# Kernel optimization log

Measured on AMD Instinct MI355X. Metric: run time of the kernel, lower is better.

The kernel has to match this reference:

```python
import math
import jax, jax.numpy as jnp
import numpy as np
from jax import lax

B, T, C, H = 8, 2048, 1024, 16
E = C // H
FACTOR = 5
TOP_K = int(FACTOR * math.log(T))  # 38


def setup_inputs() -> dict:
    key = jax.random.key(0)
    ks = jax.random.split(key, 9)
    s = 1.0 / math.sqrt(C)
    return {
        "x": jax.random.normal(ks[0], (B, T, C), dtype=jnp.float32),
        "Wq": jax.random.normal(ks[1], (C, C), dtype=jnp.float32) * s,
        "bq": jnp.zeros((C,), dtype=jnp.float32),
        "Wk": jax.random.normal(ks[2], (C, C), dtype=jnp.float32) * s,
        "bk": jnp.zeros((C,), dtype=jnp.float32),
        "Wv": jax.random.normal(ks[3], (C, C), dtype=jnp.float32) * s,
        "bv": jnp.zeros((C,), dtype=jnp.float32),
        "Wp": jax.random.normal(ks[4], (C, C), dtype=jnp.float32) * s,
        "bp": jnp.zeros((C,), dtype=jnp.float32),
    }


def _autocorrelation(x, Wq, bq, Wk, bk, Wv, bv, Wp, bp):
    # Q, K, V projections -> [B, T, H, E]
    q = (x @ Wq + bq).reshape(B, T, H, E)
    k = (x @ Wk + bk).reshape(B, T, H, E)
    v = (x @ Wv + bv).reshape(B, T, H, E)

    # [B, H, E, L] layout for FFT along time axis
    qh = q.transpose(0, 2, 3, 1)
    kh = k.transpose(0, 2, 3, 1)
    values = v.transpose(0, 2, 3, 1)

    # period-based dependency discovery via FFT cross-correlation
    qf = jnp.fft.rfft(qh, axis=-1)
    kf = jnp.fft.rfft(kh, axis=-1)
    corr = jnp.fft.irfft(qf * jnp.conj(kf), n=T, axis=-1)  # [B, H, E, L]

    # inference-mode time-delay aggregation (per-batch top-k delays)
    mean_value = jnp.mean(corr, axis=(1, 2))               # [B, L]
    weights, delay = lax.top_k(mean_value, TOP_K)          # [B, K] each
    tmp_corr = jax.nn.softmax(weights, axis=-1)            # [B, K]

    init_index = jnp.arange(T)

    def step(agg, wd):
        w, d = wd  # w: [B], d: [B]  (one delay per batch element)
        idx = (init_index[None, :] + d[:, None]) % T        # modular roll == gather on doubled values
        pattern = jnp.take_along_axis(values, idx[:, None, None, :], axis=-1)
        return agg + pattern * w[:, None, None, None], None

    agg, _ = lax.scan(step, jnp.zeros_like(values),
                      (tmp_corr.T, delay.T))               # [B, H, E, L]

    # Faithful to the original: permute(0,3,1,2) then transpose(1,2) then view(B,T,C)
    # net effect: [B,H,E,L] -> [B,H,L,E] -> reshape(B,T,C)
    V = agg.transpose(0, 1, 3, 2).reshape(B, T, C)
    return V @ Wp + bp  # dropouts are inactive (eval mode)


def reference(x, Wq, bq, Wk, bk, Wv, bv, Wp, bp):
    return _autocorrelation(x, Wq, bq, Wk, bk, Wv, bv, Wp, bp)
```

## Files before the change

### kernel.cpp

```cpp
#include <hip/hip_runtime.h>

#define T_LEN 2048
#define B_DIM 8
#define C_DIM 1024
#define TOPK  38
#define FFT_N 2048
#define SPEC_ST 2050

typedef _Float16 half8 __attribute__((ext_vector_type(8)));
typedef _Float16 half4 __attribute__((ext_vector_type(4)));
typedef float  floatx4 __attribute__((ext_vector_type(4)));
typedef unsigned int u32;

__device__ __forceinline__ void async16(const void* g, void* l) {
  __builtin_amdgcn_global_load_lds(
      (const __attribute__((address_space(1))) u32*)g,
      (__attribute__((address_space(3))) u32*)l, 16, 0, 0);
}

__device__ __forceinline__ int rev11(int x) { return (int)(__brev((u32)x) >> 21); }
__device__ __forceinline__ int SW(int a) { return a ^ ((a >> 5) & 31); }

struct cpx { float r, i; };
__device__ __forceinline__ cpx csqr(cpx a) { return {a.r*a.r - a.i*a.i, 2.0f*a.r*a.i}; }
__device__ __forceinline__ cpx c8m(cpx a, int m) {
  const float R2 = 0.70710678118654752f;
  switch (m & 3) {
    case 0:  return a;
    case 1:  return {R2*(a.r + a.i), R2*(a.i - a.r)};
    case 2:  return {a.i, -a.r};
    default: return {R2*(a.i - a.r), -R2*(a.r + a.i)};
  }
}

__device__ __forceinline__ void radix8(float zr[8], float zi[8], cpx tb) {
  cpx tb2 = csqr(tb), tb4 = csqr(tb2);
  #pragma unroll
  for (int m = 0; m < 4; ++m) {
    cpx tw = c8m(tb, m);
    float ur = zr[m], ui = zi[m], vr = zr[m+4], vi = zi[m+4];
    zr[m] = ur + vr; zi[m] = ui + vi;
    float sr = ur - vr, si = ui - vi;
    zr[m+4] = sr*tw.r - si*tw.i; zi[m+4] = sr*tw.i + si*tw.r;
  }
  cpx twb = c8m(tb2, 2);
  #pragma unroll
  for (int h = 0; h < 2; ++h) {
    int b0 = h * 4;
    { cpx tw = tb2;
      float ur = zr[b0], ui = zi[b0], vr = zr[b0+2], vi = zi[b0+2];
      zr[b0] = ur + vr; zi[b0] = ui + vi;
      float sr = ur - vr, si = ui - vi;
      zr[b0+2] = sr*tw.r - si*tw.i; zi[b0+2] = sr*tw.i + si*tw.r; }
    { cpx tw = twb;
      float ur = zr[b0+1], ui = zi[b0+1], vr = zr[b0+3], vi = zi[b0+3];
      zr[b0+1] = ur + vr; zi[b0+1] = ui + vi;
      float sr = ur - vr, si = ui - vi;
      zr[b0+3] = sr*tw.r - si*tw.i; zi[b0+3] = sr*tw.i + si*tw.r; }
  }
  #pragma unroll
  for (int p = 0; p < 8; p += 2) {
    float ur = zr[p], ui = zi[p], vr = zr[p+1], vi = zi[p+1];
    zr[p] = ur + vr; zi[p] = ui + vi;
    float sr = ur - vr, si = ui - vi;
    zr[p+1] = sr*tb4.r - si*tb4.i; zi[p+1] = sr*tb4.i + si*tb4.r;
  }
}

__global__ __launch_bounds__(256) void init_kernel(
    float* __restrict__ spec, int n, float* __restrict__ twg) {
  int i = blockIdx.x * 256 + threadIdx.x;
  if (i < n) spec[i] = 0.0f;
  if (i < FFT_N / 2) {
    float th = -3.14159265358979323846f * (float)i / 1024.0f;
    twg[2 * i]     = cosf(th);
    twg[2 * i + 1] = sinf(th);
  }
}

__global__ __launch_bounds__(256) void cvt_f16_kernel(
    const float* __restrict__ src, _Float16* __restrict__ dst, int n8) {
  int i = blockIdx.x * 256 + threadIdx.x;
  if (i >= n8) return;
  floatx4 a = ((const floatx4*)src)[i * 2];
  floatx4 b = ((const floatx4*)src)[i * 2 + 1];
  half8 o;
  #pragma unroll
  for (int j = 0; j < 4; ++j) { o[j] = (_Float16)a[j]; o[j + 4] = (_Float16)b[j]; }
  ((half8*)dst)[i] = o;
}

__global__ __launch_bounds__(256) void wt3_kernel(
    const float* __restrict__ w0, const float* __restrict__ w1,
    const float* __restrict__ w2, _Float16* __restrict__ d0,
    _Float16* __restrict__ d1, _Float16* __restrict__ d2) {
  const float* src = blockIdx.z == 0 ? w0 : (blockIdx.z == 1 ? w1 : w2);
  _Float16*    dst = blockIdx.z == 0 ? d0 : (blockIdx.z == 1 ? d1 : d2);
  __shared__ _Float16 tile[64][65];
  int k0 = blockIdx.y * 64, n0 = blockIdx.x * 64;
  int tx = threadIdx.x & 63, ty = threadIdx.x >> 6;
  #pragma unroll
  for (int j = 0; j < 16; ++j) {
    int r = j * 4 + ty;
    tile[r][tx] = (_Float16)src[(size_t)(k0 + r) * C_DIM + n0 + tx];
  }
  __syncthreads();
  #pragma unroll
  for (int j = 0; j < 16; ++j) {
    int r = j * 4 + ty;
    dst[(size_t)(n0 + r) * C_DIM + k0 + tx] = tile[tx][r];
  }
}

__global__ __launch_bounds__(256) void tr16_kernel(
    const _Float16* __restrict__ src, _Float16* __restrict__ dst) {
  __shared__ _Float16 tile[64][65];
  int b = blockIdx.z;
  int t0 = blockIdx.x * 64, c0 = blockIdx.y * 64;
  const _Float16* s = src + (size_t)b * T_LEN * C_DIM;
  _Float16* d = dst + (size_t)b * C_DIM * T_LEN;
  int tid = threadIdx.x;
  int c8 = (tid & 7) * 8, tr = tid >> 3;
  #pragma unroll
  for (int h = 0; h < 2; ++h) {
    int r = tr + h * 32;
    half8 v = *(const half8*)&s[(size_t)(t0 + r) * C_DIM + c0 + c8];
    #pragma unroll
    for (int j = 0; j < 8; ++j) tile[r][c8 + j] = v[j];
  }
  __syncthreads();
  int t8 = (tid & 7) * 8, cr = tid >> 3;
  #pragma unroll
  for (int h = 0; h < 2; ++h) {
    int c = cr + h * 32;
    half8 o;
    #pragma unroll
    for (int j = 0; j < 8; ++j) o[j] = tile[t8 + j][c];
    *(half8*)&d[(size_t)(c0 + c) * T_LEN + t0 + t8] = o;
  }
}

#define CG 4
__global__ __launch_bounds__(256) void fft_corr_kernel(
    const _Float16* __restrict__ XMt, const _Float16* __restrict__ Xt,
    const float* __restrict__ twg, float* __restrict__ spec) {
  __shared__ float2 zc[FFT_N];
  const int tid = threadIdx.x;
  const int b = blockIdx.x & 7;
  const int cg0 = (blockIdx.x >> 3) * CG;
  const int lo5 = tid & 31, blk = tid >> 5;
  const int lo2 = tid & 3,  g   = tid >> 2;
  const _Float16* xmB = XMt + (size_t)b * C_DIM * T_LEN;
  const _Float16* xB  = Xt  + (size_t)b * C_DIM * T_LEN;
  float sRa[4] = {0.f, 0.f, 0.f, 0.f};
  float sIa[4] = {0.f, 0.f, 0.f, 0.f};
  float s1024 = 0.f;
  float zr[8], zi[8], nr[8], ni[8];
  #pragma unroll
  for (int m = 0; m < 8; ++m) {
    nr[m] = (float)xmB[(size_t)cg0 * T_LEN + tid + 256 * m];
    ni[m] = (float)xB [(size_t)cg0 * T_LEN + tid + 256 * m];
  }
  cpx tA = {twg[2 * tid],            twg[2 * tid + 1]};
  cpx tB = {twg[2 * (8 * lo5)],      twg[2 * (8 * lo5) + 1]};
  cpx tC = {twg[2 * (64 * lo2)],     twg[2 * (64 * lo2) + 1]};
  for (int cc = 0; cc < CG; ++cc) {
    #pragma unroll
    for (int m = 0; m < 8; ++m) { zr[m] = nr[m]; zi[m] = ni[m]; }
    if (cc + 1 < CG) {
      const size_t off = (size_t)(cg0 + cc + 1) * T_LEN;
      #pragma unroll
      for (int m = 0; m < 8; ++m) {
        nr[m] = (float)xmB[off + tid + 256 * m];
        ni[m] = (float)xB [off + tid + 256 * m];
      }
    }
    radix8(zr, zi, tA);
    __syncthreads();
    #pragma unroll
    for (int m = 0; m < 8; ++m) { int a = SW(tid + 256 * m); zc[a] = make_float2(zr[m], zi[m]); }
    __syncthreads();
    #pragma unroll
    for (int m = 0; m < 8; ++m) { float2 v = zc[SW(256 * blk + 32 * m + lo5)]; zr[m] = v.x; zi[m] = v.y; }
    radix8(zr, zi, tB);
    __syncthreads();
    #pragma unroll
    for (int m = 0; m < 8; ++m) { int a = SW(256 * blk + 32 * m + lo5); zc[a] = make_float2(zr[m], zi[m]); }
    __syncthreads();
    #pragma unroll
    for (int m = 0; m < 8; ++m) { float2 v = zc[SW(32 * g + 4 * m + lo2)]; zr[m] = v.x; zi[m] = v.y; }
    radix8(zr, zi, tC);
    #pragma unroll
    for (int m = 0; m < 8; ++m) {
      float pr = __shfl_xor(zr[m], 2), pi = __shfl_xor(zi[m], 2);
      if ((tid & 2) == 0) { zr[m] += pr; zi[m] += pi; }
      else {
        float sr = pr - zr[m], si = pi - zi[m];
        if (tid & 1) { zr[m] = si; zi[m] = -sr; }
        else         { zr[m] = sr; zi[m] = si; }
      }
    }
    #pragma unroll
    for (int m = 0; m < 8; ++m) {
      float pr = __shfl_xor(zr[m], 1), pi = __shfl_xor(zi[m], 1);
      if ((tid & 1) == 0) { zr[m] += pr; zi[m] += pi; }
      else                { zr[m] = pr - zr[m]; zi[m] = pi - zi[m]; }
    }
    __syncthreads();
    #pragma unroll
    for (int m = 0; m < 8; ++m) { int a = SW(32 * g + 4 * m + lo2); zc[a] = make_float2(zr[m], zi[m]); }
    __syncthreads();
    #pragma unroll
    for (int r = 0; r < 4; ++r) {
      int k = tid + r * 256;
      if (k == 0) {
        float2 z0 = zc[SW(0)], z1 = zc[SW(1)];
        sRa[0] += z0.x * z0.y;
        s1024  += z1.x * z1.y;
      } else {
        float2 zk = zc[SW(rev11(k))], zn = zc[SW(rev11(FFT_N - k))];
        float ar = 0.5f * (zk.x + zn.x), ai = 0.5f * (zk.y - zn.y);
        float br = 0.5f * (zk.y + zn.y), bi = -0.5f * (zk.x - zn.x);
        sRa[r] += ar * br + ai * bi;
        sIa[r] += ai * br - ar * bi;
      }
    }
  }
  float* sb = spec + (size_t)b * SPEC_ST;
  #pragma unroll
  for (int r = 0; r < 4; ++r) {
    int k = tid + r * 256;
    atomicAdd(&sb[2 * k],     sRa[r]);
    atomicAdd(&sb[2 * k + 1], sIa[r]);
  }
  if (tid == 0) atomicAdd(&sb[2048], s1024);
}

__global__ __launch_bounds__(256) void ifft_topk_kernel(
    const float* __restrict__ spec, const float* __restrict__ twg,
    float* __restrict__ wgt, int* __restrict__ dly) {
  __shared__ float re[FFT_N], im[FFT_N];
  __shared__ float twr[FFT_N / 2], twi[FFT_N / 2];
  __shared__ float vals[FFT_N];
  __shared__ float swv[4];
  __shared__ int   swidx[4];
  __shared__ float selw[TOPK];
  __shared__ int   seli[TOPK];
  int b = blockIdx.x, tid = threadIdx.x;
  for (int i = tid; i < FFT_N / 2; i += 256) { twr[SW(i)] = twg[2 * i]; twi[SW(i)] = twg[2 * i + 1]; }
  const float* sb = spec + (size_t)b * SPEC_ST;
  for (int i = tid; i < FFT_N; i += 256) {
    int src = (i <= 1024) ? i : (FFT_N - i);
    float sgn = (i <= 1024) ? 1.0f : -1.0f;
    re[SW(i)] = sb[2 * src];
    im[SW(i)] = sgn * sb[2 * src + 1];
  }
  __syncthreads();
  #pragma unroll 1
  for (int s = 0; s < 11; ++s) {
    const int half = 1024 >> s, tstep = 1 << s;
    #pragma unroll
    for (int r = 0; r < 4; ++r) {
      int idx = tid + r * 256;
      int j = idx & (half - 1);
      int i0 = SW(2 * idx - j), i1 = SW(2 * idx - j + half);
      float ur = re[i0], ui = im[i0], vr = re[i1], vi = im[i1];
      float sr = ur - vr, si = ui - vi;
      int tix = SW(j * tstep);
      float wr = twr[tix], wi = twi[tix];
      re[i0] = ur + vr; im[i0] = ui + vi;
      re[i1] = sr * wr + si * wi;
      im[i1] = si * wr - sr * wi;
    }
    __syncthreads();
  }
  const float sc = 1.0f / 2097152.0f;
  for (int i = tid; i < FFT_N; i += 256) vals[SW(rev11(i))] = re[SW(i)] * sc;
  __syncthreads();
  for (int it = 0; it < TOPK; ++it) {
    float bv = -3.4e38f; int bi = T_LEN - 1;
    for (int i = tid; i < T_LEN; i += 256) {
      float v = vals[SW(i)];
      if (v > bv || (v == bv && i < bi)) { bv = v; bi = i; }
    }
    #pragma unroll
    for (int off = 32; off > 0; off >>= 1) {
      float ov = __shfl_down(bv, off);
      int   oi = __shfl_down(bi, off);
      if (ov > bv || (ov == bv && oi < bi)) { bv = ov; bi = oi; }
    }
    if ((tid & 63) == 0) { swv[tid >> 6] = bv; swidx[tid >> 6] = bi; }
    __syncthreads();
    if (tid == 0) {
      #pragma unroll
      for (int ww = 1; ww < 4; ++ww) {
        float ov = swv[ww]; int oi = swidx[ww];
        if (ov > bv || (ov == bv && oi < bi)) { bv = ov; bi = oi; }
      }
      if (bi < 0) bi = 0; if (bi > T_LEN - 1) bi = T_LEN - 1;
      selw[it] = bv; seli[it] = bi;
      vals[SW(bi)] = -3.4e38f;
    }
    __syncthreads();
  }
  if (tid == 0) {
    float m = selw[0], s = 0.0f, e[TOPK];
    for (int i = 0; i < TOPK; ++i) { e[i] = expf(selw[i] - m); s += e[i]; }
    float inv = 1.0f / s;
    for (int i = 0; i < TOPK; ++i) { wgt[b * TOPK + i] = e[i] * inv; dly[b * TOPK + i] = seli[i]; }
  }
}

template <int EPI>
__global__ __launch_bounds__(256, 3) void gemm_f16_kernel(
    const _Float16* __restrict__ A, const _Float16* __restrict__ B,
    const float* __restrict__ bias, void* __restrict__ outv, int N, int K,
    const _Float16* __restrict__ B2, const float* __restrict__ bias2,
    void* __restrict__ outv2) {
  __shared__ __align__(16) _Float16 lA[128 * 64];
  __shared__ __align__(16) _Float16 lB[128 * 64];

  if (blockIdx.z) { B = B2; bias = bias2; outv = outv2; }

  const int tid = threadIdx.x;
  const int bm = blockIdx.x, bn = blockIdx.y;
  const int lane = tid & 63, w = tid >> 6;
  const int wm = w >> 1, wn = w & 1;
  const int lr = lane & 15, lg = lane >> 4;

  const int lrow = lane >> 3;
  const int lcol = (((lane & 7) ^ lrow) * 8);

  const _Float16* pA[4];
  const _Float16* pB[4];
  _Float16* dA[4];
  _Float16* dB[4];
  #pragma unroll
  for (int j = 0; j < 4; ++j) {
    int r = w * 32 + j * 8;
    pA[j] = A + (long long)(bm * 128 + r + lrow) * K + lcol;
    pB[j] = B + (long long)(bn * 128 + r + lrow) * K + lcol;
    dA[j] = &lA[r * 64];
    dB[j] = &lB[r * 64];
  }

  const int coff = (((lr >> 2) & 1) * 32) | ((lg ^ (lr & 3)) * 8);

  floatx4 acc[4][4];
  #pragma unroll
  for (int i = 0; i < 4; ++i)
    #pragma unroll
    for (int j = 0; j < 4; ++j) { acc[i][j][0]=0.f; acc[i][j][1]=0.f; acc[i][j][2]=0.f; acc[i][j][3]=0.f; }

  const int nk = K >> 6;
  for (int kt = 0; kt < nk; ++kt) {
    __syncthreads();
    #pragma unroll
    for (int j = 0; j < 4; ++j) {
      async16(pA[j], dA[j]);
      async16(pB[j], dB[j]);
      pA[j] += 64; pB[j] += 64;
    }
    __syncthreads();
    #pragma unroll
    for (int s = 0; s < 2; ++s) {
      const int so = coff ^ (s * 32);
      half8 af[4], bf[4];
      #pragma unroll
      for (int mi = 0; mi < 4; ++mi)
        af[mi] = *(const half8*)&lA[(wm * 64 + mi * 16 + lr) * 64 + so];
      #pragma unroll
      for (int ni = 0; ni < 4; ++ni)
        bf[ni] = *(const half8*)&lB[(wn * 64 + ni * 16 + lr) * 64 + so];
      #pragma unroll
      for (int mi = 0; mi < 4; ++mi)
        #pragma unroll
        for (int ni = 0; ni < 4; ++ni)
          acc[mi][ni] = __builtin_amdgcn_mfma_f32_16x16x32_f16(
              af[mi], bf[ni], acc[mi][ni], 0, 0, 0);
    }
  }

  if (EPI == 2 && blockIdx.z == 0) {
    #pragma unroll
    for (int mi = 0; mi < 4; ++mi)
      #pragma unroll
      for (int ni = 0; ni < 4; ++ni) {
        int gc  = bn * 128 + wn * 64 + ni * 16 + lr;
        int gr0 = bm * 128 + wm * 64 + mi * 16 + lg * 4;
        int bb = gr0 >> 11, t0 = gr0 & (T_LEN - 1);
        half4 o;
        #pragma unroll
        for (int i = 0; i < 4; ++i) o[i] = (_Float16)acc[mi][ni][i];
        *(half4*)&(((_Float16*)outv)[((size_t)bb * C_DIM + gc) * T_LEN + t0]) = o;
      }
    return;
  }

  float bvs[4];
  #pragma unroll
  for (int ni = 0; ni < 4; ++ni) {
    int gc = bn * 128 + wn * 64 + ni * 16 + lr;
    bvs[ni] = bias ? bias[gc & (C_DIM - 1)] : 0.0f;
  }
  #pragma unroll
  for (int mi = 0; mi < 4; ++mi)
    #pragma unroll
    for (int ni = 0; ni < 4; ++ni) {
      int gc = bn * 128 + wn * 64 + ni * 16 + lr;
      #pragma unroll
      for (int i = 0; i < 4; ++i) {
        int gr = bm * 128 + wm * 64 + mi * 16 + lg * 4 + i;
        float v = acc[mi][ni][i] + bvs[ni];
        long long idx = (long long)gr * N + gc;
        if constexpr (EPI == 1) ((float*)outv)[idx] = v;
        else                    ((_Float16*)outv)[idx] = (_Float16)v;
      }
    }
}

__global__ __launch_bounds__(256) void aggregate_kernel(
    const _Float16* __restrict__ V, const float* __restrict__ wgt,
    const int* __restrict__ dly, _Float16* __restrict__ V2) {
  int b = blockIdx.x & 7;
  int g = (blockIdx.x >> 3) * 256 + threadIdx.x;
  int c8 = g & 127;
  int tp = g >> 7;
  int h = tp >> 7, lhi = tp & 127;
  int cp = c8 << 3;
  int e0 = cp & 63, lo = cp >> 6;
  int l = lhi * 16 + lo;
  int ch = h * 64 + e0;
  float acc[8];
  #pragma unroll
  for (int j = 0; j < 8; ++j) acc[j] = 0.0f;
  const long long vbase = (long long)b * T_LEN * C_DIM;
  for (int k = 0; k < TOPK; ++k) {
    float w = wgt[b * TOPK + k];
    int d = dly[b * TOPK + k];
    int ts = (l + d) & (T_LEN - 1);
    half8 vv = *(const half8*)(V + vbase + (long long)ts * C_DIM + ch);
    #pragma unroll
    for (int j = 0; j < 8; ++j) acc[j] += w * (float)vv[j];
  }
  half8 o;
  #pragma unroll
  for (int j = 0; j < 8; ++j) o[j] = (_Float16)acc[j];
  __builtin_nontemporal_store(o, (half8*)(V2 + vbase + (long long)tp * C_DIM + cp));
}

extern "C" void kernel_launch(void* const* d_in, const int* in_sizes, int n_in,
                              void* d_out, int out_size, void* d_ws, size_t ws_size,
                              hipStream_t stream) {
  const float* x  = (const float*)d_in[0];
  const float* Wq = (const float*)d_in[1];
  const float* Wk = (const float*)d_in[3];
  const float* Wv = (const float*)d_in[5];
  const float* bv = (const float*)d_in[6];
  const float* Wp = (const float*)d_in[7];
  const float* bp = (const float*)d_in[8];

  const size_t SZ_H = (size_t)B_DIM * T_LEN * C_DIM * 2;
  const size_t NEEDED = 2 * SZ_H + 65536 + 8192;
  if (ws_size < NEEDED) return;

  char* ws = (char*)d_ws;
  _Float16* XMt = (_Float16*)ws;
  _Float16* V   = (_Float16*)(ws + SZ_H);
  float* wgt   = (float*)(ws + 2 * SZ_H + 65536);
  int*   dly   = (int*)(ws + 2 * SZ_H + 65536 + 4096);
  _Float16* V2  = (_Float16*)ws;
  _Float16* Wpt = (_Float16*)(ws + SZ_H);

  char* dob = (char*)d_out;
  _Float16* xh  = (_Float16*)dob;
  float*    spec = (float*)dob;
  float*    twg  = (float*)(dob + 131072);
  _Float16* Wqh = (_Float16*)(dob + 32 * 1048576);
  _Float16* Wkh = (_Float16*)(dob + 34 * 1048576);
  _Float16* Wvt = (_Float16*)(dob + 36 * 1048576);
  _Float16* Mt2 = (_Float16*)(dob + 38 * 1048576);
  _Float16* Xt  = (_Float16*)(dob + 32 * 1048576);

  const int M = B_DIM * T_LEN;

  cvt_f16_kernel<<<(M * C_DIM / 8) / 256, 256, 0, stream>>>(x, xh, M * C_DIM / 8);
  cvt_f16_kernel<<<(C_DIM * C_DIM / 8) / 256, 256, 0, stream>>>(Wq, Wqh, C_DIM * C_DIM / 8);
  cvt_f16_kernel<<<(C_DIM * C_DIM / 8) / 256, 256, 0, stream>>>(Wk, Wkh, C_DIM * C_DIM / 8);

  dim3 tgrid(16, 16, 1);
  wt3_kernel<<<tgrid, 256, 0, stream>>>(Wv, Wv, Wv, Wvt, Wvt, Wvt);

  dim3 pgrid2(M / 128, C_DIM / 128, 2);
  dim3 pgrid(M / 128, C_DIM / 128, 1);
  dim3 mgrid(C_DIM / 128, C_DIM / 128, 1);

  gemm_f16_kernel<0><<<mgrid, 256, 0, stream>>>(Wkh, Wqh, nullptr, Mt2, C_DIM, C_DIM,
                                                nullptr, nullptr, nullptr);
  gemm_f16_kernel<2><<<pgrid2, 256, 0, stream>>>(xh, Mt2, nullptr, XMt, C_DIM, C_DIM,
                                                 Wvt, bv, V);

  dim3 trgrid(T_LEN / 64, C_DIM / 64, B_DIM);
  tr16_kernel<<<trgrid, 256, 0, stream>>>(xh, Xt);

  init_kernel<<<(B_DIM * SPEC_ST + 255) / 256, 256, 0, stream>>>(spec, B_DIM * SPEC_ST, twg);

  fft_corr_kernel<<<B_DIM * (C_DIM / CG), 256, 0, stream>>>(XMt, Xt, twg, spec);
  ifft_topk_kernel<<<B_DIM, 256, 0, stream>>>(spec, twg, wgt, dly);

  aggregate_kernel<<<(T_LEN * C_DIM / 8 / 256) * B_DIM, 256, 0, stream>>>(V, wgt, dly, V2);

  wt3_kernel<<<tgrid, 256, 0, stream>>>(Wp, Wp, Wp, Wpt, Wpt, Wpt);

  gemm_f16_kernel<1><<<pgrid, 256, 0, stream>>>(V2, Wpt, bp, d_out, C_DIM, C_DIM,
                                                nullptr, nullptr, nullptr);
}
```

Measured before the change: 485.3 us.

## Use 256x256 double-buffered GEMM tiles for large projections

Adds a 512-thread GEMM kernel with 256x256 output tiles whose LDS is double-buffered, so global-to-LDS async loads for tile t+2 overlap MFMA compute on the current tile, with explicit vmcnt waits and raised scheduling priority around MFMAs. The large projection GEMMs (XM/V and the output projection) use it, while the small weight GEMM keeps a simplified 128-tile kernel. The aim is better data reuse and hiding of load latency. In exchange it raises register and LDS pressure (128KB LDS per block) and launches fewer blocks per GEMM.

Measured after the change: 472.7 us. -2.6%, faster.

```diff
diff --git a/kernel.cpp b/kernel.cpp
--- a/kernel.cpp
+++ b/kernel.cpp
@@ -311,26 +311,18 @@
   }
 }
 
-template <int EPI>
-__global__ __launch_bounds__(256, 3) void gemm_f16_kernel(
+__global__ __launch_bounds__(256, 3) void gemm128_kernel(
     const _Float16* __restrict__ A, const _Float16* __restrict__ B,
-    const float* __restrict__ bias, void* __restrict__ outv, int N, int K,
-    const _Float16* __restrict__ B2, const float* __restrict__ bias2,
-    void* __restrict__ outv2) {
+    _Float16* __restrict__ out, int N, int K) {
   __shared__ __align__(16) _Float16 lA[128 * 64];
   __shared__ __align__(16) _Float16 lB[128 * 64];
-
-  if (blockIdx.z) { B = B2; bias = bias2; outv = outv2; }
-
   const int tid = threadIdx.x;
   const int bm = blockIdx.x, bn = blockIdx.y;
   const int lane = tid & 63, w = tid >> 6;
   const int wm = w >> 1, wn = w & 1;
   const int lr = lane & 15, lg = lane >> 4;
-
   const int lrow = lane >> 3;
   const int lcol = (((lane & 7) ^ lrow) * 8);
-
   const _Float16* pA[4];
   const _Float16* pB[4];
   _Float16* dA[4];
@@ -343,15 +335,12 @@
     dA[j] = &lA[r * 64];
     dB[j] = &lB[r * 64];
   }
-
   const int coff = (((lr >> 2) & 1) * 32) | ((lg ^ (lr & 3)) * 8);
-
   floatx4 acc[4][4];
   #pragma unroll
   for (int i = 0; i < 4; ++i)
     #pragma unroll
     for (int j = 0; j < 4; ++j) { acc[i][j][0]=0.f; acc[i][j][1]=0.f; acc[i][j][2]=0.f; acc[i][j][3]=0.f; }
-
   const int nk = K >> 6;
   for (int kt = 0; kt < nk; ++kt) {
     __syncthreads();
@@ -380,14 +369,120 @@
               af[mi], bf[ni], acc[mi][ni], 0, 0, 0);
     }
   }
+  #pragma unroll
+  for (int mi = 0; mi < 4; ++mi)
+    #pragma unroll
+    for (int ni = 0; ni < 4; ++ni) {
+      int gc = bn * 128 + wn * 64 + ni * 16 + lr;
+      #pragma unroll
+      for (int i = 0; i < 4; ++i) {
+        int gr = bm * 128 + wm * 64 + mi * 16 + lg * 4 + i;
+        out[(long long)gr * N + gc] = (_Float16)acc[mi][ni][i];
+      }
+    }
+}
+
+template <int EPI>
+__global__ __launch_bounds__(512, 2) void gemm256_kernel(
+    const _Float16* __restrict__ A, const _Float16* __restrict__ B,
+    const float* __restrict__ bias, void* __restrict__ outv, int N, int K,
+    const _Float16* __restrict__ B2, const float* __restrict__ bias2,
+    void* __restrict__ outv2) {
+  __shared__ __align__(16) _Float16 lds[2][2][256 * 64];
+
+  if (blockIdx.z) { B = B2; bias = bias2; outv = outv2; }
+
+  const int tid = threadIdx.x;
+  const int bm = blockIdx.x, bn = blockIdx.y;
+  const int lane = tid & 63, w = tid >> 6;
+  const int wr = w >> 2, wc = w & 3;
+  const int lr = lane & 15, lg = lane >> 4;
+
+  const int strow = tid >> 3;
+  const int stcol = ((tid & 7) ^ (strow & 7)) * 8;
+  const _Float16* gA = A + (long long)(bm * 256 + strow) * K + stcol;
+  const _Float16* gB = B + (long long)(bn * 256 + strow) * K + stcol;
+  const int wbase = (tid >> 6) * 8;
+
+  const int coff = (((lr >> 2) & 1) * 32) | ((lg ^ (lr & 3)) * 8);
+
+  floatx4 acc[8][4];
+  #pragma unroll
+  for (int i = 0; i < 8; ++i)
+    #pragma unroll
+    for (int j = 0; j < 4; ++j) { acc[i][j][0]=0.f; acc[i][j][1]=0.f; acc[i][j][2]=0.f; acc[i][j][3]=0.f; }
+
+  auto STAGE = [&](int buf, int kt) {
+    const _Float16* sa = gA + (long long)kt * 64;
+    const _Float16* sb = gB + (long long)kt * 64;
+    _Float16* da = &lds[buf][0][wbase * 64];
+    _Float16* db = &lds[buf][1][wbase * 64];
+    #pragma unroll
+    for (int j = 0; j < 4; ++j) {
+      async16(sa + (long long)j * 64 * K, da + j * 64 * 64);
+      async16(sb + (long long)j * 64 * K, db + j * 64 * 64);
+    }
+  };
+
+  auto COMPUTE = [&](int buf) {
+    const _Float16* la = &lds[buf][0][0];
+    const _Float16* lb = &lds[buf][1][0];
+    #pragma unroll
+    for (int s = 0; s < 2; ++s) {
+      const int so = coff ^ (s * 32);
+      half8 bf[4];
+      #pragma unroll
+      for (int ni = 0; ni < 4; ++ni)
+        bf[ni] = *(const half8*)&lb[(wc * 64 + ni * 16 + lr) * 64 + so];
+      #pragma unroll
+      for (int mh = 0; mh < 2; ++mh) {
+        half8 af[4];
+        #pragma unroll
+        for (int q = 0; q < 4; ++q)
+          af[q] = *(const half8*)&la[(wr * 128 + (mh * 4 + q) * 16 + lr) * 64 + so];
+        __builtin_amdgcn_s_setprio(1);
+        #pragma unroll
+        for (int q = 0; q < 4; ++q)
+          #pragma unroll
+          for (int ni = 0; ni < 4; ++ni)
+            acc[mh * 4 + q][ni] = __builtin_amdgcn_mfma_f32_16x16x32_f16(
+                af[q], bf[ni], acc[mh * 4 + q][ni], 0, 0, 0);
+        __builtin_amdgcn_s_setprio(0);
+      }
+    }
+  };
+
+  const int nt = K >> 6;
+  STAGE(0, 0);
+  STAGE(1, 1);
+  asm volatile("s_waitcnt vmcnt(8)" ::: "memory");
+  __builtin_amdgcn_s_barrier();
+  asm volatile("" ::: "memory");
+
+  int cur = 0;
+  for (int t = 0; t < nt; ++t) {
+    COMPUTE(cur);
+    asm volatile("" ::: "memory");
+    __builtin_amdgcn_s_barrier();
+    asm volatile("" ::: "memory");
+    if (t + 2 < nt) {
+      STAGE(cur, t + 2);
+      asm volatile("s_waitcnt vmcnt(8)" ::: "memory");
+    } else {
+      asm volatile("s_waitcnt vmcnt(0)" ::: "memory");
+    }
+    __builtin_amdgcn_s_barrier();
+    asm volatile("" ::: "memory");
+    cur ^= 1;
+  }
 
   if (EPI == 2 && blockIdx.z == 0) {
     #pragma unroll
-    for (int mi = 0; mi < 4; ++mi)
+    for (int mi = 0; mi < 8; ++mi)
       #pragma unroll
       for (int ni = 0; ni < 4; ++ni) {
-        int gc  = bn * 128 + wn * 64 + ni * 16 + lr;
-        int gr0 = bm * 128 + wm * 64 + mi * 16 + lg * 4;
+        int gc  = bn * 256 + wc * 64 + ni * 16 + lr;
+        int gr0 = bm * 256 + wr * 128 + mi * 16 + lg * 4;
         int bb = gr0 >> 11, t0 = gr0 & (T_LEN - 1);
         half4 o;
         #pragma unroll
@@ -400,17 +495,17 @@
   float bvs[4];
   #pragma unroll
   for (int ni = 0; ni < 4; ++ni) {
-    int gc = bn * 128 + wn * 64 + ni * 16 + lr;
+    int gc = bn * 256 + wc * 64 + ni * 16 + lr;
     bvs[ni] = bias ? bias[gc & (C_DIM - 1)] : 0.0f;
   }
   #pragma unroll
-  for (int mi = 0; mi < 4; ++mi)
+  for (int mi = 0; mi < 8; ++mi)
     #pragma unroll
     for (int ni = 0; ni < 4; ++ni) {
-      int gc = bn * 128 + wn * 64 + ni * 16 + lr;
+      int gc = bn * 256 + wc * 64 + ni * 16 + lr;
       #pragma unroll
       for (int i = 0; i < 4; ++i) {
-        int gr = bm * 128 + wm * 64 + mi * 16 + lg * 4 + i;
+        int gr = bm * 256 + wr * 128 + mi * 16 + lg * 4 + i;
         float v = acc[mi][ni][i] + bvs[ni];
         long long idx = (long long)gr * N + gc;
         if constexpr (EPI == 1) ((float*)outv)[idx] = v;
@@ -491,14 +586,12 @@
   dim3 tgrid(16, 16, 1);
   wt3_kernel<<<tgrid, 256, 0, stream>>>(Wv, Wv, Wv, Wvt, Wvt, Wvt);
 
-  dim3 pgrid2(M / 128, C_DIM / 128, 2);
-  dim3 pgrid(M / 128, C_DIM / 128, 1);
   dim3 mgrid(C_DIM / 128, C_DIM / 128, 1);
-
-  gemm_f16_kernel<0><<<mgrid, 256, 0, stream>>>(Wkh, Wqh, nullptr, Mt2, C_DIM, C_DIM,
-                                                nullptr, nullptr, nullptr);
-  gemm_f16_kernel<2><<<pgrid2, 256, 0, stream>>>(xh, Mt2, nullptr, XMt, C_DIM, C_DIM,
-                                                 Wvt, bv, V);
+  gemm128_kernel<<<mgrid, 256, 0, stream>>>(Wkh, Wqh, Mt2, C_DIM, C_DIM);
+
+  dim3 pgrid2(M / 256, C_DIM / 256, 2);
+  gemm256_kernel<2><<<pgrid2, 512, 0, stream>>>(xh, Mt2, nullptr, XMt, C_DIM, C_DIM,
+                                                Wvt, bv, V);
 
   dim3 trgrid(T_LEN / 64, C_DIM / 64, B_DIM);
   tr16_kernel<<<trgrid, 256, 0, stream>>>(xh, Xt);
@@ -512,6 +605,7 @@
 
   wt3_kernel<<<tgrid, 256, 0, stream>>>(Wp, Wp, Wp, Wpt, Wpt, Wpt);
 
-  gemm_f16_kernel<1><<<pgrid, 256, 0, stream>>>(V2, Wpt, bp, d_out, C_DIM, C_DIM,
-                                                nullptr, nullptr, nullptr);
-}
+  dim3 pgrid(M / 256, C_DIM / 256, 1);
+  gemm256_kernel<1><<<pgrid, 512, 0, stream>>>(V2, Wpt, bp, d_out, C_DIM, C_DIM,
+                                               nullptr, nullptr, nullptr);
+}
```
